# Kernel optimization log

Measured on AMD Instinct MI355X. Metric: run time of the kernel, lower is better.

The kernel has to match this reference:

```python
import jax, jax.numpy as jnp
import numpy as np

MARGIN = 1.0


def setup_inputs() -> dict:
    key = jax.random.key(0)
    k1, k2 = jax.random.split(key)
    B, D, K = 2048, 256, 8
    scores = jax.random.normal(k1, (B, D), dtype=jnp.float32)
    pos_indices = jax.random.randint(k2, (B, K), 0, D, dtype=jnp.int64)
    return {"scores": scores, "pos_indices": pos_indices, "num_developers": D}


def reference(scores, pos_indices, num_developers):
    B, D = scores.shape
    # boolean positive mask per sample (duplicate indices collapse like a set)
    pos_mask = jnp.zeros((B, D), dtype=scores.dtype)
    pos_mask = pos_mask.at[jnp.arange(B)[:, None], pos_indices].set(1.0)
    neg_mask = 1.0 - pos_mask
    # all-pairs hinge: relu(s_neg - s_pos + margin), masked to (neg, pos) pairs
    # diff[b, n, p] = scores[b, n] - scores[b, p] + margin
    diff = scores[:, :, None] - scores[:, None, :] + MARGIN
    pair_mask = neg_mask[:, :, None] * pos_mask[:, None, :]
    loss_sum = jnp.sum(jax.nn.relu(diff) * pair_mask)
    num_pairs = jnp.sum(pair_mask)
    # original returns 0.0 when there are no (pos, neg) pairs
    return jnp.where(num_pairs > 0, loss_sum / jnp.maximum(num_pairs, 1.0), 0.0)
```

## Files before the change

kernel.cpp:

```cpp
#include <hip/hip_runtime.h>

#define TPB 256
#define NBLK 512

template <int KC>
__device__ inline void accum_samples(const float* __restrict__ scores,
                                     const int* __restrict__ idx,
                                     int D, int B, int K,
                                     float& loss, float& pairs) {
    const int KK = (KC > 0) ? KC : K;
    for (int b = blockIdx.x; b < B; b += gridDim.x) {
        const int rbase = b * D;
        const int ibase = b * K;

        if (KC > 0) {
            int   ik[KC > 0 ? KC : 1];
            float ps[KC > 0 ? KC : 1];
            int   validmask = 0, P = 0;
#pragma unroll
            for (int k = 0; k < KC; ++k) ik[k] = idx[ibase + k];
#pragma unroll
            for (int k = 0; k < KC; ++k) {
                bool dup = false;
#pragma unroll
                for (int j = 0; j < KC; ++j)
                    if (j < k) dup |= (ik[j] == ik[k]);
                if (!dup) { validmask |= (1 << k); ++P; }
                ps[k] = scores[rbase + ik[k]];
            }
            for (int d = threadIdx.x; d < D; d += TPB) {
                const float s = scores[rbase + d] + 1.0f;
                bool is_pos = false;
#pragma unroll
                for (int k = 0; k < KC; ++k) is_pos |= (ik[k] == d);
                if (!is_pos) {
#pragma unroll
                    for (int k = 0; k < KC; ++k) {
                        if (validmask & (1 << k)) {
                            float v = s - ps[k];
                            loss += (v > 0.0f) ? v : 0.0f;
                        }
                    }
                }
            }
            if (threadIdx.x == 0) pairs += (float)((D - P) * P);
        } else {
            int P = 0;
            for (int k = 0; k < KK; ++k) {
                bool dup = false;
                for (int j = 0; j < k; ++j) dup |= (idx[ibase + j] == idx[ibase + k]);
                if (!dup) ++P;
            }
            for (int d = threadIdx.x; d < D; d += TPB) {
                const float s = scores[rbase + d] + 1.0f;
                bool is_pos = false;
                for (int k = 0; k < KK; ++k) is_pos |= (idx[ibase + k] == d);
                if (!is_pos) {
                    for (int k = 0; k < KK; ++k) {
                        bool dup = false;
                        for (int j = 0; j < k; ++j) dup |= (idx[ibase + j] == idx[ibase + k]);
                        if (!dup) {
                            float v = s - scores[rbase + idx[ibase + k]];
                            loss += (v > 0.0f) ? v : 0.0f;
                        }
                    }
                }
            }
            if (threadIdx.x == 0) pairs += (float)((D - P) * P);
        }
    }
}

__global__ __launch_bounds__(TPB) void mlrl_fused(
        const float* __restrict__ scores,
        const int* __restrict__ idx,
        const int* __restrict__ ndev,
        int total_scores, int total_idx,
        unsigned int* __restrict__ counter,
        float2* __restrict__ partials,
        float* __restrict__ out) {
    const int D = *ndev;
    const int B = total_scores / D;
    const int K = total_idx / B;

    float loss = 0.0f, pairs = 0.0f;
    if (K == 8) accum_samples<8>(scores, idx, D, B, K, loss, pairs);
    else        accum_samples<0>(scores, idx, D, B, K, loss, pairs);

    for (int off = 32; off > 0; off >>= 1) {
        loss  += __shfl_down(loss,  off);
        pairs += __shfl_down(pairs, off);
    }
    __shared__ float2 red[TPB / 64];
    __shared__ bool   amLast;
    const int wave = threadIdx.x >> 6;
    const int lane = threadIdx.x & 63;
    if (lane == 0) red[wave] = make_float2(loss, pairs);
    __syncthreads();
    if (threadIdx.x == 0) {
        float2 acc = red[0];
        for (int w = 1; w < TPB / 64; ++w) { acc.x += red[w].x; acc.y += red[w].y; }
        partials[blockIdx.x] = acc;
        __threadfence();
        unsigned int old = atomicAdd(counter, 1u);
        amLast = (old == (unsigned int)gridDim.x - 1u);
    }
    __syncthreads();

    if (amLast) {
        __threadfence();
        double l = 0.0, p = 0.0;
        for (int i = threadIdx.x; i < (int)gridDim.x; i += TPB) {
            float2 v = partials[i];
            l += (double)v.x;
            p += (double)v.y;
        }
        for (int off = 32; off > 0; off >>= 1) {
            l += __shfl_down(l, off);
            p += __shfl_down(p, off);
        }
        __shared__ double sl[TPB / 64], sp[TPB / 64];
        if (lane == 0) { sl[wave] = l; sp[wave] = p; }
        __syncthreads();
        if (threadIdx.x == 0) {
            double L = 0.0, P = 0.0;
            for (int w = 0; w < TPB / 64; ++w) { L += sl[w]; P += sp[w]; }
            out[0] = (P > 0.0) ? (float)(L / (P < 1.0 ? 1.0 : P)) : 0.0f;
        }
    }
}

extern "C" void kernel_launch(void* const* d_in, const int* in_sizes, int n_in,
                              void* d_out, int out_size, void* d_ws, size_t ws_size,
                              hipStream_t stream) {
    const float* scores = (const float*)d_in[0];
    const int*   idx    = (const int*)d_in[1];
    const int*   ndev   = (const int*)d_in[2];
    float* out = (float*)d_out;

    const int total_scores = in_sizes[0];
    const int total_idx    = in_sizes[1];

    unsigned int* counter  = (unsigned int*)d_ws;
    float2*       partials = (float2*)((char*)d_ws + 16);

    hipMemsetAsync(d_ws, 0, 4, stream);

    mlrl_fused<<<NBLK, TPB, 0, stream>>>(scores, idx, ndev,
                                         total_scores, total_idx,
                                         counter, partials, out);
}
```

Baseline: 74.59 us.

## Split reduction into main and finalize kernels, drop memset and atomic counter

Replaces the last-block-done pattern (memset, threadfence, atomic counter) with two kernel launches: a main kernel writing per-block partials and a single-block finalize kernel. The grid grows from 512 to total_scores/256 blocks (2048 here), one sample per block. This removes the memset launch and the fence/atomic serialization, but adds a second kernel launch and more block scheduling overhead.

```diff
diff --git a/kernel.cpp b/kernel.cpp
--- a/kernel.cpp
+++ b/kernel.cpp
@@ -1,14 +1,12 @@
 #include <hip/hip_runtime.h>
 
 #define TPB 256
-#define NBLK 512
 
 template <int KC>
 __device__ inline void accum_samples(const float* __restrict__ scores,
                                      const int* __restrict__ idx,
                                      int D, int B, int K,
                                      float& loss, float& pairs) {
-    const int KK = (KC > 0) ? KC : K;
     for (int b = blockIdx.x; b < B; b += gridDim.x) {
         const int rbase = b * D;
         const int ibase = b * K;
@@ -46,7 +44,7 @@
             if (threadIdx.x == 0) pairs += (float)((D - P) * P);
         } else {
             int P = 0;
-            for (int k = 0; k < KK; ++k) {
+            for (int k = 0; k < K; ++k) {
                 bool dup = false;
                 for (int j = 0; j < k; ++j) dup |= (idx[ibase + j] == idx[ibase + k]);
                 if (!dup) ++P;
@@ -54,9 +52,9 @@
             for (int d = threadIdx.x; d < D; d += TPB) {
                 const float s = scores[rbase + d] + 1.0f;
                 bool is_pos = false;
-                for (int k = 0; k < KK; ++k) is_pos |= (idx[ibase + k] == d);
+                for (int k = 0; k < K; ++k) is_pos |= (idx[ibase + k] == d);
                 if (!is_pos) {
-                    for (int k = 0; k < KK; ++k) {
+                    for (int k = 0; k < K; ++k) {
                         bool dup = false;
                         for (int j = 0; j < k; ++j) dup |= (idx[ibase + j] == idx[ibase + k]);
                         if (!dup) {
@@ -71,14 +69,12 @@
     }
 }
 
-__global__ __launch_bounds__(TPB) void mlrl_fused(
+__global__ __launch_bounds__(TPB) void mlrl_main(
         const float* __restrict__ scores,
         const int* __restrict__ idx,
         const int* __restrict__ ndev,
         int total_scores, int total_idx,
-        unsigned int* __restrict__ counter,
-        float2* __restrict__ partials,
-        float* __restrict__ out) {
+        float2* __restrict__ partials) {
     const int D = *ndev;
     const int B = total_scores / D;
     const int K = total_idx / B;
@@ -92,7 +88,6 @@
         pairs += __shfl_down(pairs, off);
     }
     __shared__ float2 red[TPB / 64];
-    __shared__ bool   amLast;
     const int wave = threadIdx.x >> 6;
     const int lane = threadIdx.x & 63;
     if (lane == 0) red[wave] = make_float2(loss, pairs);
@@ -101,32 +96,30 @@
         float2 acc = red[0];
         for (int w = 1; w < TPB / 64; ++w) { acc.x += red[w].x; acc.y += red[w].y; }
         partials[blockIdx.x] = acc;
-        __threadfence();
-        unsigned int old = atomicAdd(counter, 1u);
-        amLast = (old == (unsigned int)gridDim.x - 1u);
     }
+}
+
+__global__ __launch_bounds__(TPB) void mlrl_finalize(
+        const float2* __restrict__ partials, int n, float* __restrict__ out) {
+    double l = 0.0, p = 0.0;
+    for (int i = threadIdx.x; i < n; i += blockDim.x) {
+        float2 v = partials[i];
+        l += (double)v.x;
+        p += (double)v.y;
+    }
+    for (int off = 32; off > 0; off >>= 1) {
+        l += __shfl_down(l, off);
+        p += __shfl_down(p, off);
+    }
+    __shared__ double sl[TPB / 64], sp[TPB / 64];
+    const int wave = threadIdx.x >> 6;
+    const int lane = threadIdx.x & 63;
+    if (lane == 0) { sl[wave] = l; sp[wave] = p; }
     __syncthreads();
-
-    if (amLast) {
-        __threadfence();
-        double l = 0.0, p = 0.0;
-        for (int i = threadIdx.x; i < (int)gridDim.x; i += TPB) {
-            float2 v = partials[i];
-            l += (double)v.x;
-            p += (double)v.y;
-        }
-        for (int off = 32; off > 0; off >>= 1) {
-            l += __shfl_down(l, off);
-            p += __shfl_down(p, off);
-        }
-        __shared__ double sl[TPB / 64], sp[TPB / 64];
-        if (lane == 0) { sl[wave] = l; sp[wave] = p; }
-        __syncthreads();
-        if (threadIdx.x == 0) {
-            double L = 0.0, P = 0.0;
-            for (int w = 0; w < TPB / 64; ++w) { L += sl[w]; P += sp[w]; }
-            out[0] = (P > 0.0) ? (float)(L / (P < 1.0 ? 1.0 : P)) : 0.0f;
-        }
+    if (threadIdx.x == 0) {
+        double L = 0.0, P = 0.0;
+        for (int w = 0; w < TPB / 64; ++w) { L += sl[w]; P += sp[w]; }
+        out[0] = (P > 0.0) ? (float)(L / (P < 1.0 ? 1.0 : P)) : 0.0f;
     }
 }
 
@@ -141,12 +134,14 @@
     const int total_scores = in_sizes[0];
     const int total_idx    = in_sizes[1];
 
-    unsigned int* counter  = (unsigned int*)d_ws;
-    float2*       partials = (float2*)((char*)d_ws + 16);
+    int nblocks = total_scores / 256;
+    if (nblocks < 1) nblocks = 1;
+    if ((size_t)nblocks * sizeof(float2) > ws_size)
+        nblocks = (int)(ws_size / sizeof(float2));
 
-    hipMemsetAsync(d_ws, 0, 4, stream);
+    float2* partials = (float2*)d_ws;
 
-    mlrl_fused<<<NBLK, TPB, 0, stream>>>(scores, idx, ndev,
-                                         total_scores, total_idx,
-                                         counter, partials, out);
+    mlrl_main<<<nblocks, TPB, 0, stream>>>(scores, idx, ndev,
+                                           total_scores, total_idx, partials);
+    mlrl_finalize<<<1, TPB, 0, stream>>>(partials, nblocks, out);
 }
```

Measured after the change: 63.90 us. 14.3% less time.
